# Performance work log

Measured on AMD Instinct MI355X. Metric: run time of the kernel, lower is better.

The kernel has to match this reference:

```python
import jax, jax.numpy as jnp
import numpy as np

B, T, D, H, E, M = 4, 2048, 2048, 8, 512, 8  # batch, seq, hidden, moe_heads, moe_experts, moe_dim//2
F = E * M  # flatten_shape = 4096
HALF = D // 2


def act(z):
    # 'relu2' activation: relu(x)**2
    r = jax.nn.relu(z)
    return r * r


def setup_inputs() -> dict:
    key = jax.random.key(0)
    ks = jax.random.split(key, 13)
    s = 0.02
    return {
        "x": jax.random.normal(ks[0], (B, T, D), jnp.float32),
        "g1": jax.random.uniform(ks[1], (B, T, H, E), jnp.float32),
        "g2": jax.random.uniform(ks[2], (B, T, H, E), jnp.float32),
        "u1_w": jax.random.normal(ks[3], (F, D), jnp.float32) * s,
        "u1_b": jnp.zeros((F,), jnp.float32),
        "u2_w": jax.random.normal(ks[4], (F, D), jnp.float32) * s,
        "u2_b": jnp.zeros((F,), jnp.float32),
        "v11_w": jax.random.normal(ks[5], (HALF, F), jnp.float32) * s,
        "v12_w": jax.random.normal(ks[6], (HALF, F), jnp.float32) * s,
        "v21_w": jax.random.normal(ks[7], (HALF, F), jnp.float32) * s,
        "v22_w": jax.random.normal(ks[8], (HALF, F), jnp.float32) * s,
        "b1": jax.random.normal(ks[9], (E, HALF), jnp.float32) * s,
        "b2": jax.random.normal(ks[10], (E, HALF), jnp.float32) * s,
    }


def reference(x, g1, g2, u1_w, u1_b, u2_w, u2_b, v11_w, v12_w, v21_w, v22_w, b1, b2):
    # x1, x2: [B,T,E,M]
    x1 = act(x @ u1_w.T + u1_b).reshape(B, T, E, M)
    x2 = act(x @ u2_w.T + u2_b).reshape(B, T, E, M)

    g1s = g1.sum(axis=2)  # [B,T,E] (einsum '...hi->...i')
    g2s = g2.sum(axis=2)

    # x11 = v11(einsum('btim,bthi->btim', x1, g1).flatten(-2))
    x11 = (x1 * g1s[..., None]).reshape(B, T, F) @ v11_w.T
    # x12 = v12(einsum('btjm,bthj,bthi->btim', x2, g2, g1).flatten(-2))
    t2 = jnp.einsum('btjm,bthj->bthm', x2, g2)
    x12 = jnp.einsum('bthm,bthi->btim', t2, g1).reshape(B, T, F) @ v12_w.T
    # x13 = einsum('bthi,id->btd', g1, b1)
    x13 = g1s @ b1

    # x21 = v21(einsum('btim,bthi,bthj->btjm', x1, g1, g2).flatten(-2))
    t1 = jnp.einsum('btim,bthi->bthm', x1, g1)
    x21 = jnp.einsum('bthm,bthj->btjm', t1, g2).reshape(B, T, F) @ v21_w.T
    # x22 = v22(einsum('btjm,bthj->btjm', x2, g2).flatten(-2))
    x22 = (x2 * g2s[..., None]).reshape(B, T, F) @ v22_w.T
    # x23 = einsum('bthj,jd->btd', g2, b2)
    x23 = g2s @ b2

    return jnp.concatenate((x11 + x12 + x13, x21 + x22 + x23), axis=-1)
```

## Files before the change

kernel.cpp:

```cpp
#include <hip/hip_runtime.h>
#include <hip/hip_bf16.h>

#define TOK   8192
#define DD    2048
#define FF    4096
#define EE    512
#define HALF  1024
#define KCAT  8704

typedef __bf16 bf16x8 __attribute__((ext_vector_type(8)));
typedef __bf16 bf16x4 __attribute__((ext_vector_type(4)));
typedef float  f32x4  __attribute__((ext_vector_type(4)));
using bf16 = __hip_bfloat16;

#define AS1(p) ((const __attribute__((address_space(1))) void*)(p))
#define AS3(p) ((__attribute__((address_space(3))) void*)(p))


__global__ void cvt_bf16(const float* __restrict__ in, bf16* __restrict__ out, int n4) {
    int i = blockIdx.x * blockDim.x + threadIdx.x;
    int stride = gridDim.x * blockDim.x;
    for (; i < n4; i += stride) {
        float4 v = ((const float4*)in)[i];
        bf16x4 o;
        o[0] = (__bf16)v.x; o[1] = (__bf16)v.y; o[2] = (__bf16)v.z; o[3] = (__bf16)v.w;
        ((bf16x4*)out)[i] = o;
    }
}

__global__ void pack_w(const float* __restrict__ vA, const float* __restrict__ vB,
                       const float* __restrict__ bmat, bf16* __restrict__ W) {
    int n = blockIdx.x;
    const float* ra = vA + (size_t)n * FF;
    const float* rb = vB + (size_t)n * FF;
    bf16* w = W + (size_t)n * KCAT;
    for (int k = threadIdx.x; k < FF; k += 256) {
        w[k]      = __float2bfloat16(ra[k]);
        w[FF + k] = __float2bfloat16(rb[k]);
    }
    for (int e = threadIdx.x; e < EE; e += 256)
        w[2 * FF + e] = __float2bfloat16(bmat[(size_t)e * HALF + n]);
}

template<int MODE>
__global__ __launch_bounds__(512, 2)
void gemmP(const bf16* __restrict__ A0, const bf16* __restrict__ B0,
           const float* __restrict__ bias0, void* __restrict__ C0,
           const bf16* __restrict__ A1, const bf16* __restrict__ B1,
           const float* __restrict__ bias1, void* __restrict__ C1,
           int nbm, int nbn, int K, int ldc)
{
    __shared__ __align__(16) char smem[131072];
    const int tid  = threadIdx.x;
    const int lane = tid & 63;
    const int wid  = tid >> 6;
    const int wm = wid >> 2, wn = wid & 3;
    const int r16 = lane & 15, kb = lane >> 4;

    int bid = blockIdx.x;
    {
        int nwg = gridDim.x;
        int q = nwg >> 3, r = nwg & 7;
        int xcd = bid & 7, idx = bid >> 3;
        bid = (xcd < r ? xcd * (q + 1) : r * (q + 1) + (xcd - r) * q) + idx;
    }
    const int npg = nbm * nbn;
    const int g   = bid / npg;
    const int lb  = bid - g * npg;
    const int bm = lb / nbn, bn = lb - bm * nbn;

    const bf16*  A    = g ? A1 : A0;
    const bf16*  Bw   = g ? B1 : B0;
    const float* bias = g ? bias1 : bias0;
    char* Cout = (char*)(g ? C1 : C0);

    const long row0 = (long)bm * 256;
    const int  col0 = bn * 256;
    const int  nt   = K >> 6;

    const char* gA[2]; const char* gB[2];
    #pragma unroll
    for (int l = 0; l < 2; ++l) {
        const uint32_t S = (uint32_t)(l * 512 + tid) * 16;
        const int r  = (int)(S >> 6);
        const int cb = (int)((S & 63) ^ ((uint32_t)((r >> 1) & 3) << 4));
        gA[l] = (const char*)A  + (row0 + r) * (long)K * 2 + cb;
        gB[l] = (const char*)Bw + (long)(col0 + r) * K * 2 + cb;
    }
    const uint32_t ldst = (uint32_t)(tid & ~63) * 16;

    const uint32_t swz  = ((uint32_t)(r16 >> 1) & 3u) << 4;
    const uint32_t aoff = (uint32_t)((wm * 128 + r16) * 64 + kb * 16) ^ swz;
    const uint32_t boff = (uint32_t)((wn * 64  + r16) * 64 + kb * 16) ^ swz;

    f32x4 acc[8][4];
    #pragma unroll
    for (int i = 0; i < 8; ++i)
        #pragma unroll
        for (int j = 0; j < 4; ++j)
            acc[i][j] = (f32x4){0.f, 0.f, 0.f, 0.f};

    __builtin_amdgcn_global_load_lds(AS1(gA[0]),      AS3(smem +     0 + ldst), 16, 0, 0);
    __builtin_amdgcn_global_load_lds(AS1(gA[1]),      AS3(smem +  8192 + ldst), 16, 0, 0);
    __builtin_amdgcn_global_load_lds(AS1(gB[0]),      AS3(smem + 32768 + ldst), 16, 0, 0);
    __builtin_amdgcn_global_load_lds(AS1(gB[1]),      AS3(smem + 40960 + ldst), 16, 0, 0);
    __builtin_amdgcn_global_load_lds(AS1(gA[0] + 64), AS3(smem + 16384 + ldst), 16, 0, 0);
    __builtin_amdgcn_global_load_lds(AS1(gA[1] + 64), AS3(smem + 24576 + ldst), 16, 0, 0);
    __builtin_amdgcn_global_load_lds(AS1(gB[0] + 64), AS3(smem + 49152 + ldst), 16, 0, 0);
    __builtin_amdgcn_global_load_lds(AS1(gB[1] + 64), AS3(smem + 57344 + ldst), 16, 0, 0);
    asm volatile("s_waitcnt vmcnt(4)\n\ts_barrier" ::: "memory");

#define MFMA16(IH)                                                                       \
    __builtin_amdgcn_s_setprio(1);                                                      \
    _Pragma("unroll")                                                                    \
    for (int fi = 0; fi < 4; ++fi) {                                                     \
        acc[(IH)*4+fi][0] = __builtin_amdgcn_mfma_f32_16x16x32_bf16(af[fi], bv[0], acc[(IH)*4+fi][0], 0, 0, 0); \
        acc[(IH)*4+fi][1] = __builtin_amdgcn_mfma_f32_16x16x32_bf16(af[fi], bv[1], acc[(IH)*4+fi][1], 0, 0, 0); \
        acc[(IH)*4+fi][2] = __builtin_amdgcn_mfma_f32_16x16x32_bf16(af[fi], bv[2], acc[(IH)*4+fi][2], 0, 0, 0); \
        acc[(IH)*4+fi][3] = __builtin_amdgcn_mfma_f32_16x16x32_bf16(af[fi], bv[3], acc[(IH)*4+fi][3], 0, 0, 0); \
    }                                                                                    \
    __builtin_amdgcn_s_setprio(0);

    for (int t = 0; t < nt; ++t) {
        const char* pb = smem + (t & 1) * 65536;
        char*       pt = smem + ((t + 1) & 1) * 65536;
        const bool  st = (t + 1 < nt);
        const long  koff = (long)(t + 1) * 128;

        bf16x8 af[4], bv[4];

        #pragma unroll
        for (int fj = 0; fj < 4; ++fj) bv[fj] = *(const bf16x8*)(pb + 32768 + boff + fj * 1024);
        #pragma unroll
        for (int fi = 0; fi < 4; ++fi) af[fi] = *(const bf16x8*)(pb + aoff + fi * 1024);
        if (st) {
            __builtin_amdgcn_global_load_lds(AS1(gA[0] + koff), AS3(pt +    0 + ldst), 16, 0, 0);
            __builtin_amdgcn_global_load_lds(AS1(gA[1] + koff), AS3(pt + 8192 + ldst), 16, 0, 0);
        }
        asm volatile("s_barrier" ::: "memory");
        MFMA16(0)
        asm volatile("s_barrier" ::: "memory");

        #pragma unroll
        for (int fi = 0; fi < 4; ++fi) af[fi] = *(const bf16x8*)(pb + 4096 + aoff + fi * 1024);
        if (st) {
            __builtin_amdgcn_global_load_lds(AS1(gB[0] + koff), AS3(pt + 32768 + ldst), 16, 0, 0);
            __builtin_amdgcn_global_load_lds(AS1(gB[1] + koff), AS3(pt + 40960 + ldst), 16, 0, 0);
            asm volatile("s_waitcnt vmcnt(4)" ::: "memory");
        } else {
            asm volatile("s_waitcnt vmcnt(0)" ::: "memory");
        }
        asm volatile("s_barrier" ::: "memory");
        MFMA16(1)
        asm volatile("s_barrier" ::: "memory");

        #pragma unroll
        for (int fj = 0; fj < 4; ++fj) bv[fj] = *(const bf16x8*)(pb + 49152 + boff + fj * 1024);
        #pragma unroll
        for (int fi = 0; fi < 4; ++fi) af[fi] = *(const bf16x8*)(pb + 16384 + aoff + fi * 1024);
        if (st) {
            __builtin_amdgcn_global_load_lds(AS1(gA[0] + koff + 64), AS3(pt + 16384 + ldst), 16, 0, 0);
            __builtin_amdgcn_global_load_lds(AS1(gA[1] + koff + 64), AS3(pt + 24576 + ldst), 16, 0, 0);
        }
        asm volatile("s_barrier" ::: "memory");
        MFMA16(0)
        asm volatile("s_barrier" ::: "memory");

        #pragma unroll
        for (int fi = 0; fi < 4; ++fi) af[fi] = *(const bf16x8*)(pb + 16384 + 4096 + aoff + fi * 1024);
        if (st) {
            __builtin_amdgcn_global_load_lds(AS1(gB[0] + koff + 64), AS3(pt + 49152 + ldst), 16, 0, 0);
            __builtin_amdgcn_global_load_lds(AS1(gB[1] + koff + 64), AS3(pt + 57344 + ldst), 16, 0, 0);
            asm volatile("s_waitcnt vmcnt(4)" ::: "memory");
        }
        asm volatile("s_barrier" ::: "memory");
        MFMA16(1)
        asm volatile("s_barrier" ::: "memory");
    }
#undef MFMA16

    const int rb = (lane >> 4) * 4;
    #pragma unroll
    for (int i = 0; i < 8; ++i) {
        #pragma unroll
        for (int j = 0; j < 4; ++j) {
            const int cc = col0 + wn * 64 + j * 16 + r16;
            float badd = 0.f;
            if (MODE == 1) badd = bias[cc];
            #pragma unroll
            for (int e = 0; e < 4; ++e) {
                long row = row0 + wm * 128 + i * 16 + rb + e;
                float v = acc[i][j][e];
                if (MODE == 1) {
                    v += badd;
                    v = fmaxf(v, 0.f);
                    v = v * v;
                    ((bf16*)Cout)[row * ldc + cc] = __float2bfloat16(v);
                } else {
                    ((float*)Cout)[row * ldc + cc] = v;
                }
            }
        }
    }
}

#define GPAD 524
__global__ __launch_bounds__(256)
void glue(const float* __restrict__ g1, const float* __restrict__ g2,
          bf16* __restrict__ Yl, bf16* __restrict__ Yr)
{
    __shared__ __align__(16) float g1t[8 * GPAD];
    __shared__ __align__(16) float g2t[8 * GPAD];
    __shared__ float g1s[EE], g2s[EE];
    __shared__ float t1s[64], t2s[64];
    __shared__ float t1p[4][64], t2p[4][64];
    __shared__ __align__(16) bf16 x1t[FF], x2t[FF];

    const int t   = blockIdx.x;
    const int tid = threadIdx.x;
    const float* g1p = g1 + (size_t)t * FF;
    const float* g2p = g2 + (size_t)t * FF;
    bf16* ylp = Yl + (size_t)t * KCAT;
    bf16* yrp = Yr + (size_t)t * KCAT;

    #pragma unroll
    for (int c = 0; c < 4; ++c) {
        int idx4 = (c * 256 + tid) * 4;
        float4 v1 = *(const float4*)(g1p + idx4);
        float4 v2 = *(const float4*)(g2p + idx4);
        int h = idx4 >> 9, e = idx4 & 511;
        *(float4*)&g1t[h * GPAD + e] = v1;
        *(float4*)&g2t[h * GPAD + e] = v2;
    }
    #pragma unroll
    for (int c = 0; c < 2; ++c) {
        int idx8 = (c * 256 + tid) * 8;
        *(bf16x8*)&x1t[idx8] = *(const bf16x8*)(ylp + idx8);
        *(bf16x8*)&x2t[idx8] = *(const bf16x8*)(yrp + FF + idx8);
    }
    __syncthreads();

    #pragma unroll
    for (int c = 0; c < 2; ++c) {
        int e = c * 256 + tid;
        float s1 = 0.f, s2 = 0.f;
        #pragma unroll
        for (int h = 0; h < 8; ++h) { s1 += g1t[h * GPAD + e]; s2 += g2t[h * GPAD + e]; }
        g1s[e] = s1; g2s[e] = s2;
    }

    {
        int o = tid & 63;
        int h = o & 7, m = o >> 3;
        int p = tid >> 6;
        float s1 = 0.f, s2 = 0.f;
        #pragma unroll 8
        for (int ii = 0; ii < 128; ++ii) {
            int e = p * 128 + ii;
            float xv1 = __bfloat162float(x1t[e * 8 + m]);
            float xv2 = __bfloat162float(x2t[e * 8 + m]);
            s1 += xv1 * g1t[h * GPAD + e];
            s2 += xv2 * g2t[h * GPAD + e];
        }
        t1p[p][o] = s1; t2p[p][o] = s2;
    }
    __syncthreads();
    if (tid < 64)       t1s[tid] = t1p[0][tid] + t1p[1][tid] + t1p[2][tid] + t1p[3][tid];
    else if (tid < 128) { int o = tid - 64; t2s[o] = t2p[0][o] + t2p[1][o] + t2p[2][o] + t2p[3][o]; }
    __syncthreads();

    #pragma unroll
    for (int c = 0; c < 2; ++c) {
        int f0 = (c * 256 + tid) * 8;
        int e  = f0 >> 3;
        float s1 = g1s[e], s2 = g2s[e];
        bf16x8 xa = *(const bf16x8*)&x1t[f0];
        bf16x8 xb = *(const bf16x8*)&x2t[f0];
        bf16x8 o1, o2;
        #pragma unroll
        for (int u = 0; u < 8; ++u) {
            o1[u] = (__bf16)((float)xa[u] * s1);
            o2[u] = (__bf16)((float)xb[u] * s2);
        }
        *(bf16x8*)(ylp + f0)      = o1;
        *(bf16x8*)(yrp + FF + f0) = o2;
    }
    #pragma unroll
    for (int c = 0; c < 2; ++c) {
        int f0 = (c * 256 + tid) * 8;
        int i  = f0 >> 3;
        bf16x8 o12v, o21v;
        #pragma unroll
        for (int m = 0; m < 8; ++m) {
            float s12 = 0.f, s21 = 0.f;
            #pragma unroll
            for (int h = 0; h < 8; ++h) {
                s12 += t2s[(m << 3) | h] * g1t[h * GPAD + i];
                s21 += t1s[(m << 3) | h] * g2t[h * GPAD + i];
            }
            o12v[m] = (__bf16)s12;
            o21v[m] = (__bf16)s21;
        }
        *(bf16x8*)(ylp + FF + f0) = o12v;
        *(bf16x8*)(yrp + f0)      = o21v;
    }
    {
        int e0 = tid * 2;
        ylp[2 * FF + e0]     = __float2bfloat16(g1s[e0]);
        ylp[2 * FF + e0 + 1] = __float2bfloat16(g1s[e0 + 1]);
        yrp[2 * FF + e0]     = __float2bfloat16(g2s[e0]);
        yrp[2 * FF + e0 + 1] = __float2bfloat16(g2s[e0 + 1]);
    }
}


extern "C" void kernel_launch(void* const* d_in, const int* in_sizes, int n_in,
                              void* d_out, int out_size, void* d_ws, size_t ws_size,
                              hipStream_t stream) {
    const float* x    = (const float*)d_in[0];
    const float* g1   = (const float*)d_in[1];
    const float* g2   = (const float*)d_in[2];
    const float* u1_w = (const float*)d_in[3];
    const float* u1_b = (const float*)d_in[4];
    const float* u2_w = (const float*)d_in[5];
    const float* u2_b = (const float*)d_in[6];
    const float* v11  = (const float*)d_in[7];
    const float* v12  = (const float*)d_in[8];
    const float* v21  = (const float*)d_in[9];
    const float* v22  = (const float*)d_in[10];
    const float* b1   = (const float*)d_in[11];
    const float* b2   = (const float*)d_in[12];
    float* out = (float*)d_out;

    size_t off = 0;
    char* base = (char*)d_ws;
    auto take = [&](size_t bytes) { void* p = base + off; off += (bytes + 255) & ~(size_t)255; return p; };
    bf16* Xb  = (bf16*)take((size_t)TOK * DD * 2);
    bf16* U1b = (bf16*)take((size_t)FF * DD * 2);
    bf16* U2b = (bf16*)take((size_t)FF * DD * 2);
    bf16* Wl  = (bf16*)take((size_t)HALF * KCAT * 2);
    bf16* Wr  = (bf16*)take((size_t)HALF * KCAT * 2);
    bf16* Yl  = (bf16*)take((size_t)TOK * KCAT * 2);
    bf16* Yr  = (bf16*)take((size_t)TOK * KCAT * 2);

    cvt_bf16<<<4096, 256, 0, stream>>>(x,    Xb,  TOK * DD / 4);
    cvt_bf16<<<2048, 256, 0, stream>>>(u1_w, U1b, FF * DD / 4);
    cvt_bf16<<<2048, 256, 0, stream>>>(u2_w, U2b, FF * DD / 4);
    pack_w<<<HALF, 256, 0, stream>>>(v11, v12, b1, Wl);
    pack_w<<<HALF, 256, 0, stream>>>(v21, v22, b2, Wr);

    gemmP<1><<<2 * (TOK / 256) * (FF / 256), 512, 0, stream>>>(
        Xb, U1b, u1_b, Yl,
        Xb, U2b, u2_b, Yr + FF,
        TOK / 256, FF / 256, DD, KCAT);

    glue<<<TOK, 256, 0, stream>>>(g1, g2, Yl, Yr);

    gemmP<0><<<2 * (TOK / 256) * (HALF / 256), 512, 0, stream>>>(
        Yl, Wl, nullptr, out,
        Yr, Wr, nullptr, out + HALF,
        TOK / 256, HALF / 256, KCAT, DD);
}
```

Before: 714.4 us.

## Software-pipeline LDS fragment loads against MFMA with double register buffers

The GEMM main loop now keeps two sets of A and B fragment registers. It loads the next sub-tile's fragments from LDS while MFMAs run on the current ones, and prefetches the first fragments of the next K tile at the end of each iteration. This lets it drop the barrier that used to follow each MFMA block, so LDS reads overlap matrix work and fewer sync points stall the waves. The cost is more vector registers in use and a more delicate ordering, since correctness now rests on LDS reads finishing before the async global-to-LDS writes overwrite the same buffer.

```diff
diff --git a/kernel.cpp b/kernel.cpp
--- a/kernel.cpp
+++ b/kernel.cpp
@@ -110,15 +110,22 @@
     __builtin_amdgcn_global_load_lds(AS1(gB[1] + 64), AS3(smem + 57344 + ldst), 16, 0, 0);
     asm volatile("s_waitcnt vmcnt(4)\n\ts_barrier" ::: "memory");
 
-#define MFMA16(IH)                                                                       \
+    bf16x8 afA[4], afB[4], bv0[4], bv1[4];
+    #pragma unroll
+    for (int f = 0; f < 4; ++f) {
+        afA[f] = *(const bf16x8*)(smem +     0 + aoff + f * 1024);
+        bv0[f] = *(const bf16x8*)(smem + 32768 + boff + f * 1024);
+    }
+
+#define MFMA16(AF, BV, IH)                                                              \
     __builtin_amdgcn_s_setprio(1);                                                      \
-    _Pragma("unroll")                                                                    \
-    for (int fi = 0; fi < 4; ++fi) {                                                     \
-        acc[(IH)*4+fi][0] = __builtin_amdgcn_mfma_f32_16x16x32_bf16(af[fi], bv[0], acc[(IH)*4+fi][0], 0, 0, 0); \
-        acc[(IH)*4+fi][1] = __builtin_amdgcn_mfma_f32_16x16x32_bf16(af[fi], bv[1], acc[(IH)*4+fi][1], 0, 0, 0); \
-        acc[(IH)*4+fi][2] = __builtin_amdgcn_mfma_f32_16x16x32_bf16(af[fi], bv[2], acc[(IH)*4+fi][2], 0, 0, 0); \
-        acc[(IH)*4+fi][3] = __builtin_amdgcn_mfma_f32_16x16x32_bf16(af[fi], bv[3], acc[(IH)*4+fi][3], 0, 0, 0); \
-    }                                                                                    \
+    _Pragma("unroll")                                                                   \
+    for (int fi = 0; fi < 4; ++fi) {                                                    \
+        acc[(IH)*4+fi][0] = __builtin_amdgcn_mfma_f32_16x16x32_bf16(AF[fi], BV[0], acc[(IH)*4+fi][0], 0, 0, 0); \
+        acc[(IH)*4+fi][1] = __builtin_amdgcn_mfma_f32_16x16x32_bf16(AF[fi], BV[1], acc[(IH)*4+fi][1], 0, 0, 0); \
+        acc[(IH)*4+fi][2] = __builtin_amdgcn_mfma_f32_16x16x32_bf16(AF[fi], BV[2], acc[(IH)*4+fi][2], 0, 0, 0); \
+        acc[(IH)*4+fi][3] = __builtin_amdgcn_mfma_f32_16x16x32_bf16(AF[fi], BV[3], acc[(IH)*4+fi][3], 0, 0, 0); \
+    }                                                                                   \
     __builtin_amdgcn_s_setprio(0);
 
     for (int t = 0; t < nt; ++t) {
@@ -127,22 +134,16 @@
         const bool  st = (t + 1 < nt);
         const long  koff = (long)(t + 1) * 128;
 
-        bf16x8 af[4], bv[4];
-
-        #pragma unroll
-        for (int fj = 0; fj < 4; ++fj) bv[fj] = *(const bf16x8*)(pb + 32768 + boff + fj * 1024);
-        #pragma unroll
-        for (int fi = 0; fi < 4; ++fi) af[fi] = *(const bf16x8*)(pb + aoff + fi * 1024);
         if (st) {
             __builtin_amdgcn_global_load_lds(AS1(gA[0] + koff), AS3(pt +    0 + ldst), 16, 0, 0);
             __builtin_amdgcn_global_load_lds(AS1(gA[1] + koff), AS3(pt + 8192 + ldst), 16, 0, 0);
         }
         asm volatile("s_barrier" ::: "memory");
-        MFMA16(0)
-        asm volatile("s_barrier" ::: "memory");
-
-        #pragma unroll
-        for (int fi = 0; fi < 4; ++fi) af[fi] = *(const bf16x8*)(pb + 4096 + aoff + fi * 1024);
+        #pragma unroll
+        for (int f = 0; f < 4; ++f)
+            afB[f] = *(const bf16x8*)(pb + 4096 + aoff + f * 1024);
+        MFMA16(afA, bv0, 0)
+
         if (st) {
             __builtin_amdgcn_global_load_lds(AS1(gB[0] + koff), AS3(pt + 32768 + ldst), 16, 0, 0);
             __builtin_amdgcn_global_load_lds(AS1(gB[1] + koff), AS3(pt + 40960 + ldst), 16, 0, 0);
@@ -151,31 +152,37 @@
             asm volatile("s_waitcnt vmcnt(0)" ::: "memory");
         }
         asm volatile("s_barrier" ::: "memory");
-        MFMA16(1)
-        asm volatile("s_barrier" ::: "memory");
-
-        #pragma unroll
-        for (int fj = 0; fj < 4; ++fj) bv[fj] = *(const bf16x8*)(pb + 49152 + boff + fj * 1024);
-        #pragma unroll
-        for (int fi = 0; fi < 4; ++fi) af[fi] = *(const bf16x8*)(pb + 16384 + aoff + fi * 1024);
+        #pragma unroll
+        for (int f = 0; f < 4; ++f) {
+            afA[f] = *(const bf16x8*)(pb + 16384 + aoff + f * 1024);
+            bv1[f] = *(const bf16x8*)(pb + 49152 + boff + f * 1024);
+        }
+        MFMA16(afB, bv0, 1)
+
         if (st) {
             __builtin_amdgcn_global_load_lds(AS1(gA[0] + koff + 64), AS3(pt + 16384 + ldst), 16, 0, 0);
             __builtin_amdgcn_global_load_lds(AS1(gA[1] + koff + 64), AS3(pt + 24576 + ldst), 16, 0, 0);
         }
         asm volatile("s_barrier" ::: "memory");
-        MFMA16(0)
-        asm volatile("s_barrier" ::: "memory");
-
-        #pragma unroll
-        for (int fi = 0; fi < 4; ++fi) af[fi] = *(const bf16x8*)(pb + 16384 + 4096 + aoff + fi * 1024);
+        #pragma unroll
+        for (int f = 0; f < 4; ++f)
+            afB[f] = *(const bf16x8*)(pb + 16384 + 4096 + aoff + f * 1024);
+        MFMA16(afA, bv1, 0)
+
         if (st) {
             __builtin_amdgcn_global_load_lds(AS1(gB[0] + koff + 64), AS3(pt + 49152 + ldst), 16, 0, 0);
             __builtin_amdgcn_global_load_lds(AS1(gB[1] + koff + 64), AS3(pt + 57344 + ldst), 16, 0, 0);
             asm volatile("s_waitcnt vmcnt(4)" ::: "memory");
         }
         asm volatile("s_barrier" ::: "memory");
-        MFMA16(1)
-        asm volatile("s_barrier" ::: "memory");
+        if (st) {
+            #pragma unroll
+            for (int f = 0; f < 4; ++f) {
+                afA[f] = *(const bf16x8*)(pt +     0 + aoff + f * 1024);
+                bv0[f] = *(const bf16x8*)(pt + 32768 + boff + f * 1024);
+            }
+        }
+        MFMA16(afB, bv1, 1)
     }
 #undef MFMA16
 
```

Result: faster. 692.9 us (-3.0%).

## Restructure GEMM main loop with 128-byte K rows and staggered prefetch

Applied to the files above, without the earlier changes.

Replaces the GEMM inner loop. LDS tiles now hold a full 64-wide K slice per row (128 bytes) with an 8-way XOR swizzle, and each wave covers a 128x64 quadrant split differently. Global-to-LDS staging for the next tiles is spread across the four MFMA phases, some two iterations ahead, with explicit lgkmcnt waits and sched barriers. Launch bounds drop from 2 to 1 blocks per CU to give the compiler more registers. This aims to cut LDS bank conflicts and overlap memory with compute better, at the cost of occupancy and more complex synchronisation.

```diff
diff --git a/kernel.cpp b/kernel.cpp
--- a/kernel.cpp
+++ b/kernel.cpp
@@ -43,8 +43,8 @@
 }
 
 template<int MODE>
-__global__ __launch_bounds__(512, 2)
-void gemmP(const bf16* __restrict__ A0, const bf16* __restrict__ B0,
+__global__ __launch_bounds__(512, 1)
+void gemmQ(const bf16* __restrict__ A0, const bf16* __restrict__ B0,
            const float* __restrict__ bias0, void* __restrict__ C0,
            const bf16* __restrict__ A1, const bf16* __restrict__ B1,
            const float* __restrict__ bias1, void* __restrict__ C1,
@@ -78,20 +78,31 @@
     const int  col0 = bn * 256;
     const int  nt   = K >> 6;
 
-    const char* gA[2]; const char* gB[2];
+    const char* sA[2][2]; const char* sB[2][2];
     #pragma unroll
     for (int l = 0; l < 2; ++l) {
         const uint32_t S = (uint32_t)(l * 512 + tid) * 16;
-        const int r  = (int)(S >> 6);
-        const int cb = (int)((S & 63) ^ ((uint32_t)((r >> 1) & 3) << 4));
-        gA[l] = (const char*)A  + (row0 + r) * (long)K * 2 + cb;
-        gB[l] = (const char*)Bw + (long)(col0 + r) * K * 2 + cb;
-    }
-    const uint32_t ldst = (uint32_t)(tid & ~63) * 16;
-
-    const uint32_t swz  = ((uint32_t)(r16 >> 1) & 3u) << 4;
-    const uint32_t aoff = (uint32_t)((wm * 128 + r16) * 64 + kb * 16) ^ swz;
-    const uint32_t boff = (uint32_t)((wn * 64  + r16) * 64 + kb * 16) ^ swz;
+        const int r  = (int)(S >> 7);
+        const int cs = (int)((S & 127) ^ (((uint32_t)r & 7) << 4));
+        sA[0][l] = (const char*)A  + (row0 + r)       * (long)K * 2 + cs;
+        sA[1][l] = (const char*)A  + (row0 + 128 + r) * (long)K * 2 + cs;
+        sB[0][l] = (const char*)Bw + (long)(col0 + r)       * K * 2 + cs;
+        sB[1][l] = (const char*)Bw + (long)(col0 + 128 + r) * K * 2 + cs;
+    }
+    const uint32_t dst0 = (uint32_t)(tid & ~63) * 16;
+
+#define STAGE(SP, BASE, KOFF)                                                            \
+    __builtin_amdgcn_global_load_lds(AS1(SP[0] + (KOFF)), AS3(smem + (BASE) + dst0), 16, 0, 0); \
+    __builtin_amdgcn_global_load_lds(AS1(SP[1] + (KOFF)), AS3(smem + (BASE) + 8192 + dst0), 16, 0, 0);
+
+    const uint32_t sw = ((uint32_t)(r16 & 7)) << 4;
+    uint32_t co[2];
+    co[0] = ((uint32_t)(kb * 16)) ^ sw;
+    co[1] = ((uint32_t)(64 + kb * 16)) ^ sw;
+    const uint32_t arow = (uint32_t)(r16 * 128);
+    const uint32_t brow = (uint32_t)(((wn & 1) * 64 + r16) * 128);
+    const uint32_t Ab = (uint32_t)wm * 16384u;
+    const uint32_t Bb = 32768u + ((uint32_t)(wn >> 1)) * 16384u;
 
     f32x4 acc[8][4];
     #pragma unroll
@@ -100,84 +111,90 @@
         for (int j = 0; j < 4; ++j)
             acc[i][j] = (f32x4){0.f, 0.f, 0.f, 0.f};
 
-    __builtin_amdgcn_global_load_lds(AS1(gA[0]),      AS3(smem +     0 + ldst), 16, 0, 0);
-    __builtin_amdgcn_global_load_lds(AS1(gA[1]),      AS3(smem +  8192 + ldst), 16, 0, 0);
-    __builtin_amdgcn_global_load_lds(AS1(gB[0]),      AS3(smem + 32768 + ldst), 16, 0, 0);
-    __builtin_amdgcn_global_load_lds(AS1(gB[1]),      AS3(smem + 40960 + ldst), 16, 0, 0);
-    __builtin_amdgcn_global_load_lds(AS1(gA[0] + 64), AS3(smem + 16384 + ldst), 16, 0, 0);
-    __builtin_amdgcn_global_load_lds(AS1(gA[1] + 64), AS3(smem + 24576 + ldst), 16, 0, 0);
-    __builtin_amdgcn_global_load_lds(AS1(gB[0] + 64), AS3(smem + 49152 + ldst), 16, 0, 0);
-    __builtin_amdgcn_global_load_lds(AS1(gB[1] + 64), AS3(smem + 57344 + ldst), 16, 0, 0);
-    asm volatile("s_waitcnt vmcnt(4)\n\ts_barrier" ::: "memory");
-
-#define MFMA16(IH)                                                                       \
+    STAGE(sA[0],     0, 0) STAGE(sB[0], 32768, 0) STAGE(sA[1], 16384, 0) STAGE(sB[1], 49152, 0)
+    if (nt > 1) {
+        STAGE(sA[0], 65536 +     0, 128) STAGE(sB[0], 65536 + 32768, 128) STAGE(sB[1], 65536 + 49152, 128)
+        asm volatile("s_waitcnt vmcnt(6)" ::: "memory");
+    } else {
+        asm volatile("s_waitcnt vmcnt(0)" ::: "memory");
+    }
+    asm volatile("s_barrier" ::: "memory");
+
+#define QUAD(RO, CO, AF, BV)                                                            \
     __builtin_amdgcn_s_setprio(1);                                                      \
-    _Pragma("unroll")                                                                    \
-    for (int fi = 0; fi < 4; ++fi) {                                                     \
-        acc[(IH)*4+fi][0] = __builtin_amdgcn_mfma_f32_16x16x32_bf16(af[fi], bv[0], acc[(IH)*4+fi][0], 0, 0, 0); \
-        acc[(IH)*4+fi][1] = __builtin_amdgcn_mfma_f32_16x16x32_bf16(af[fi], bv[1], acc[(IH)*4+fi][1], 0, 0, 0); \
-        acc[(IH)*4+fi][2] = __builtin_amdgcn_mfma_f32_16x16x32_bf16(af[fi], bv[2], acc[(IH)*4+fi][2], 0, 0, 0); \
-        acc[(IH)*4+fi][3] = __builtin_amdgcn_mfma_f32_16x16x32_bf16(af[fi], bv[3], acc[(IH)*4+fi][3], 0, 0, 0); \
-    }                                                                                    \
+    _Pragma("unroll")                                                                   \
+    for (int f = 0; f < 4; ++f) {                                                       \
+        _Pragma("unroll")                                                               \
+        for (int j = 0; j < 2; ++j) {                                                   \
+            acc[(RO)+f][(CO)+j] = __builtin_amdgcn_mfma_f32_16x16x32_bf16(AF[0][f], BV[0][j], acc[(RO)+f][(CO)+j], 0, 0, 0); \
+            acc[(RO)+f][(CO)+j] = __builtin_amdgcn_mfma_f32_16x16x32_bf16(AF[1][f], BV[1][j], acc[(RO)+f][(CO)+j], 0, 0, 0); \
+        }                                                                               \
+    }                                                                                   \
     __builtin_amdgcn_s_setprio(0);
 
+#define LGKM0()                                                                         \
+    asm volatile("s_waitcnt lgkmcnt(0)" ::: "memory");                                  \
+    __builtin_amdgcn_sched_barrier(0);
+
+    bf16x8 af[2][4], bv[2][2], bv2[2][2];
+
     for (int t = 0; t < nt; ++t) {
-        const char* pb = smem + (t & 1) * 65536;
-        char*       pt = smem + ((t + 1) & 1) * 65536;
-        const bool  st = (t + 1 < nt);
-        const long  koff = (long)(t + 1) * 128;
-
-        bf16x8 af[4], bv[4];
-
-        #pragma unroll
-        for (int fj = 0; fj < 4; ++fj) bv[fj] = *(const bf16x8*)(pb + 32768 + boff + fj * 1024);
-        #pragma unroll
-        for (int fi = 0; fi < 4; ++fi) af[fi] = *(const bf16x8*)(pb + aoff + fi * 1024);
-        if (st) {
-            __builtin_amdgcn_global_load_lds(AS1(gA[0] + koff), AS3(pt +    0 + ldst), 16, 0, 0);
-            __builtin_amdgcn_global_load_lds(AS1(gA[1] + koff), AS3(pt + 8192 + ldst), 16, 0, 0);
-        }
-        asm volatile("s_barrier" ::: "memory");
-        MFMA16(0)
-        asm volatile("s_barrier" ::: "memory");
-
-        #pragma unroll
-        for (int fi = 0; fi < 4; ++fi) af[fi] = *(const bf16x8*)(pb + 4096 + aoff + fi * 1024);
-        if (st) {
-            __builtin_amdgcn_global_load_lds(AS1(gB[0] + koff), AS3(pt + 32768 + ldst), 16, 0, 0);
-            __builtin_amdgcn_global_load_lds(AS1(gB[1] + koff), AS3(pt + 40960 + ldst), 16, 0, 0);
-            asm volatile("s_waitcnt vmcnt(4)" ::: "memory");
-        } else {
+        const uint32_t bo  = ((uint32_t)(t & 1)) << 16;
+        const uint32_t bo1 = bo ^ 65536u;
+        const char* pb = smem + bo;
+        const long k1 = (long)(t + 1) * 128;
+        const long k2 = (long)(t + 2) * 128;
+
+        #pragma unroll
+        for (int kk = 0; kk < 2; ++kk) {
+            #pragma unroll
+            for (int f = 0; f < 4; ++f)
+                af[kk][f] = *(const bf16x8*)(pb + Ab + arow + f * 2048 + co[kk]);
+            #pragma unroll
+            for (int j = 0; j < 2; ++j)
+                bv[kk][j] = *(const bf16x8*)(pb + Bb + brow + j * 2048 + co[kk]);
+        }
+        if (t + 1 < nt) { STAGE(sA[1], bo1 + 16384, k1) }
+        asm volatile("s_barrier" ::: "memory");
+        LGKM0()
+        QUAD(0, 0, af, bv)
+        asm volatile("s_barrier" ::: "memory");
+
+        #pragma unroll
+        for (int kk = 0; kk < 2; ++kk)
+            #pragma unroll
+            for (int j = 0; j < 2; ++j)
+                bv2[kk][j] = *(const bf16x8*)(pb + Bb + brow + (j + 2) * 2048 + co[kk]);
+        asm volatile("s_barrier" ::: "memory");
+        LGKM0()
+        QUAD(0, 2, af, bv2)
+        asm volatile("s_barrier" ::: "memory");
+
+        #pragma unroll
+        for (int kk = 0; kk < 2; ++kk)
+            #pragma unroll
+            for (int f = 0; f < 4; ++f)
+                af[kk][f] = *(const bf16x8*)(pb + Ab + arow + (f + 4) * 2048 + co[kk]);
+        if (t + 2 < nt) { STAGE(sB[0], bo + 32768, k2) }
+        asm volatile("s_barrier" ::: "memory");
+        LGKM0()
+        QUAD(4, 0, af, bv)
+        asm volatile("s_barrier" ::: "memory");
+
+        if (t + 2 < nt) {
+            STAGE(sA[0], bo, k2) STAGE(sB[1], bo + 49152, k2)
+            asm volatile("s_waitcnt vmcnt(6)" ::: "memory");
+        } else if (t + 1 < nt) {
             asm volatile("s_waitcnt vmcnt(0)" ::: "memory");
         }
         asm volatile("s_barrier" ::: "memory");
-        MFMA16(1)
-        asm volatile("s_barrier" ::: "memory");
-
-        #pragma unroll
-        for (int fj = 0; fj < 4; ++fj) bv[fj] = *(const bf16x8*)(pb + 49152 + boff + fj * 1024);
-        #pragma unroll
-        for (int fi = 0; fi < 4; ++fi) af[fi] = *(const bf16x8*)(pb + 16384 + aoff + fi * 1024);
-        if (st) {
-            __builtin_amdgcn_global_load_lds(AS1(gA[0] + koff + 64), AS3(pt + 16384 + ldst), 16, 0, 0);
-            __builtin_amdgcn_global_load_lds(AS1(gA[1] + koff + 64), AS3(pt + 24576 + ldst), 16, 0, 0);
-        }
-        asm volatile("s_barrier" ::: "memory");
-        MFMA16(0)
-        asm volatile("s_barrier" ::: "memory");
-
-        #pragma unroll
-        for (int fi = 0; fi < 4; ++fi) af[fi] = *(const bf16x8*)(pb + 16384 + 4096 + aoff + fi * 1024);
-        if (st) {
-            __builtin_amdgcn_global_load_lds(AS1(gB[0] + koff + 64), AS3(pt + 49152 + ldst), 16, 0, 0);
-            __builtin_amdgcn_global_load_lds(AS1(gB[1] + koff + 64), AS3(pt + 57344 + ldst), 16, 0, 0);
-            asm volatile("s_waitcnt vmcnt(4)" ::: "memory");
-        }
-        asm volatile("s_barrier" ::: "memory");
-        MFMA16(1)
-        asm volatile("s_barrier" ::: "memory");
-    }
-#undef MFMA16
+        __builtin_amdgcn_sched_barrier(0);
+        QUAD(4, 2, af, bv2)
+        asm volatile("s_barrier" ::: "memory");
+    }
+#undef QUAD
+#undef LGKM0
+#undef STAGE
 
     const int rb = (lane >> 4) * 4;
     #pragma unroll
@@ -349,14 +366,14 @@
     pack_w<<<HALF, 256, 0, stream>>>(v11, v12, b1, Wl);
     pack_w<<<HALF, 256, 0, stream>>>(v21, v22, b2, Wr);
 
-    gemmP<1><<<2 * (TOK / 256) * (FF / 256), 512, 0, stream>>>(
+    gemmQ<1><<<2 * (TOK / 256) * (FF / 256), 512, 0, stream>>>(
         Xb, U1b, u1_b, Yl,
         Xb, U2b, u2_b, Yr + FF,
         TOK / 256, FF / 256, DD, KCAT);
 
     glue<<<TOK, 256, 0, stream>>>(g1, g2, Yl, Yr);
 
-    gemmP<0><<<2 * (TOK / 256) * (HALF / 256), 512, 0, stream>>>(
+    gemmQ<0><<<2 * (TOK / 256) * (HALF / 256), 512, 0, stream>>>(
         Yl, Wl, nullptr, out,
         Yr, Wr, nullptr, out + HALF,
         TOK / 256, HALF / 256, KCAT, DD);
```

New measurement: 678.9 us. 1.05x faster.

## Restructure GEMM main loop into register double-buffered LDS reads with fewer barriers

Applied to the files above, without the earlier changes.

Rewrites the GEMM K-loop so each 64-wide K half-tile is read from LDS into a full 8x4 fragment set (af/bv double-buffered in registers). The next half-tile's LDS reads are issued before the MFMA block on the current one, which cuts the per-iteration barrier count from eight to two. The aim is to hide LDS latency behind MFMAs and reduce synchronisation stalls. In exchange it holds twice as many fragment registers, which could raise VGPR pressure at 512 threads with launch bounds of 2 blocks per CU.

```diff
diff --git a/kernel.cpp b/kernel.cpp
--- a/kernel.cpp
+++ b/kernel.cpp
@@ -44,7 +44,7 @@
 
 template<int MODE>
 __global__ __launch_bounds__(512, 2)
-void gemmP(const bf16* __restrict__ A0, const bf16* __restrict__ B0,
+void gemmR(const bf16* __restrict__ A0, const bf16* __restrict__ B0,
            const float* __restrict__ bias0, void* __restrict__ C0,
            const bf16* __restrict__ A1, const bf16* __restrict__ B1,
            const float* __restrict__ bias1, void* __restrict__ C1,
@@ -100,84 +100,61 @@
         for (int j = 0; j < 4; ++j)
             acc[i][j] = (f32x4){0.f, 0.f, 0.f, 0.f};
 
-    __builtin_amdgcn_global_load_lds(AS1(gA[0]),      AS3(smem +     0 + ldst), 16, 0, 0);
-    __builtin_amdgcn_global_load_lds(AS1(gA[1]),      AS3(smem +  8192 + ldst), 16, 0, 0);
-    __builtin_amdgcn_global_load_lds(AS1(gB[0]),      AS3(smem + 32768 + ldst), 16, 0, 0);
-    __builtin_amdgcn_global_load_lds(AS1(gB[1]),      AS3(smem + 40960 + ldst), 16, 0, 0);
-    __builtin_amdgcn_global_load_lds(AS1(gA[0] + 64), AS3(smem + 16384 + ldst), 16, 0, 0);
-    __builtin_amdgcn_global_load_lds(AS1(gA[1] + 64), AS3(smem + 24576 + ldst), 16, 0, 0);
-    __builtin_amdgcn_global_load_lds(AS1(gB[0] + 64), AS3(smem + 49152 + ldst), 16, 0, 0);
-    __builtin_amdgcn_global_load_lds(AS1(gB[1] + 64), AS3(smem + 57344 + ldst), 16, 0, 0);
-    asm volatile("s_waitcnt vmcnt(4)\n\ts_barrier" ::: "memory");
-
-#define MFMA16(IH)                                                                       \
-    __builtin_amdgcn_s_setprio(1);                                                      \
+#define STAGEK(BUFOFF, KOFF)                                                             \
+    __builtin_amdgcn_global_load_lds(AS1(gA[0] + (KOFF)), AS3(smem + (BUFOFF) +     0 + ldst), 16, 0, 0); \
+    __builtin_amdgcn_global_load_lds(AS1(gA[1] + (KOFF)), AS3(smem + (BUFOFF) +  8192 + ldst), 16, 0, 0); \
+    __builtin_amdgcn_global_load_lds(AS1(gB[0] + (KOFF)), AS3(smem + (BUFOFF) + 32768 + ldst), 16, 0, 0); \
+    __builtin_amdgcn_global_load_lds(AS1(gB[1] + (KOFF)), AS3(smem + (BUFOFF) + 40960 + ldst), 16, 0, 0);
+
+#define READS(AF, BV, PB, PLOFF)                                                         \
     _Pragma("unroll")                                                                    \
-    for (int fi = 0; fi < 4; ++fi) {                                                     \
-        acc[(IH)*4+fi][0] = __builtin_amdgcn_mfma_f32_16x16x32_bf16(af[fi], bv[0], acc[(IH)*4+fi][0], 0, 0, 0); \
-        acc[(IH)*4+fi][1] = __builtin_amdgcn_mfma_f32_16x16x32_bf16(af[fi], bv[1], acc[(IH)*4+fi][1], 0, 0, 0); \
-        acc[(IH)*4+fi][2] = __builtin_amdgcn_mfma_f32_16x16x32_bf16(af[fi], bv[2], acc[(IH)*4+fi][2], 0, 0, 0); \
-        acc[(IH)*4+fi][3] = __builtin_amdgcn_mfma_f32_16x16x32_bf16(af[fi], bv[3], acc[(IH)*4+fi][3], 0, 0, 0); \
+    for (int fi = 0; fi < 8; ++fi) AF[fi] = *(const bf16x8*)((PB) + (PLOFF) + aoff + fi * 1024); \
+    _Pragma("unroll")                                                                    \
+    for (int fj = 0; fj < 4; ++fj) BV[fj] = *(const bf16x8*)((PB) + (PLOFF) + 32768 + boff + fj * 1024);
+
+#define MFMA32(AF, BV)                                                                   \
+    __builtin_amdgcn_s_setprio(1);                                                       \
+    _Pragma("unroll")                                                                    \
+    for (int fi = 0; fi < 8; ++fi) {                                                     \
+        _Pragma("unroll")                                                                \
+        for (int fj = 0; fj < 4; ++fj)                                                   \
+            acc[fi][fj] = __builtin_amdgcn_mfma_f32_16x16x32_bf16(AF[fi], BV[fj], acc[fi][fj], 0, 0, 0); \
     }                                                                                    \
     __builtin_amdgcn_s_setprio(0);
 
+    STAGEK(0, 0)
+    STAGEK(16384, 64)
+    asm volatile("s_waitcnt vmcnt(4)\n\ts_barrier" ::: "memory");
+
+    bf16x8 af0[8], bv0[4], af1[8], bv1[4];
+    READS(af0, bv0, smem, 0)
+
     for (int t = 0; t < nt; ++t) {
-        const char* pb = smem + (t & 1) * 65536;
-        char*       pt = smem + ((t + 1) & 1) * 65536;
+        const uint32_t bo  = ((uint32_t)(t & 1)) << 16;
+        const uint32_t bo1 = bo ^ 65536u;
+        const char* pb = smem + bo;
+        const char* pt = smem + bo1;
         const bool  st = (t + 1 < nt);
-        const long  koff = (long)(t + 1) * 128;
-
-        bf16x8 af[4], bv[4];
-
-        #pragma unroll
-        for (int fj = 0; fj < 4; ++fj) bv[fj] = *(const bf16x8*)(pb + 32768 + boff + fj * 1024);
-        #pragma unroll
-        for (int fi = 0; fi < 4; ++fi) af[fi] = *(const bf16x8*)(pb + aoff + fi * 1024);
+        const long  k1 = (long)(t + 1) * 128;
+
+        if (st) { STAGEK(bo1, k1) }
+        if (st) asm volatile("s_waitcnt vmcnt(4)" ::: "memory");
+        else    asm volatile("s_waitcnt vmcnt(0)" ::: "memory");
+        asm volatile("s_barrier" ::: "memory");
+        READS(af1, bv1, pb, 16384)
+        MFMA32(af0, bv0)
+
         if (st) {
-            __builtin_amdgcn_global_load_lds(AS1(gA[0] + koff), AS3(pt +    0 + ldst), 16, 0, 0);
-            __builtin_amdgcn_global_load_lds(AS1(gA[1] + koff), AS3(pt + 8192 + ldst), 16, 0, 0);
+            STAGEK(bo1 + 16384, k1 + 64)
+            asm volatile("s_waitcnt vmcnt(4)" ::: "memory");
         }
         asm volatile("s_barrier" ::: "memory");
-        MFMA16(0)
-        asm volatile("s_barrier" ::: "memory");
-
-        #pragma unroll
-        for (int fi = 0; fi < 4; ++fi) af[fi] = *(const bf16x8*)(pb + 4096 + aoff + fi * 1024);
-        if (st) {
-            __builtin_amdgcn_global_load_lds(AS1(gB[0] + koff), AS3(pt + 32768 + ldst), 16, 0, 0);
-            __builtin_amdgcn_global_load_lds(AS1(gB[1] + koff), AS3(pt + 40960 + ldst), 16, 0, 0);
-            asm volatile("s_waitcnt vmcnt(4)" ::: "memory");
-        } else {
-            asm volatile("s_waitcnt vmcnt(0)" ::: "memory");
-        }
-        asm volatile("s_barrier" ::: "memory");
-        MFMA16(1)
-        asm volatile("s_barrier" ::: "memory");
-
-        #pragma unroll
-        for (int fj = 0; fj < 4; ++fj) bv[fj] = *(const bf16x8*)(pb + 49152 + boff + fj * 1024);
-        #pragma unroll
-        for (int fi = 0; fi < 4; ++fi) af[fi] = *(const bf16x8*)(pb + 16384 + aoff + fi * 1024);
-        if (st) {
-            __builtin_amdgcn_global_load_lds(AS1(gA[0] + koff + 64), AS3(pt + 16384 + ldst), 16, 0, 0);
-            __builtin_amdgcn_global_load_lds(AS1(gA[1] + koff + 64), AS3(pt + 24576 + ldst), 16, 0, 0);
-        }
-        asm volatile("s_barrier" ::: "memory");
-        MFMA16(0)
-        asm volatile("s_barrier" ::: "memory");
-
-        #pragma unroll
-        for (int fi = 0; fi < 4; ++fi) af[fi] = *(const bf16x8*)(pb + 16384 + 4096 + aoff + fi * 1024);
-        if (st) {
-            __builtin_amdgcn_global_load_lds(AS1(gB[0] + koff + 64), AS3(pt + 49152 + ldst), 16, 0, 0);
-            __builtin_amdgcn_global_load_lds(AS1(gB[1] + koff + 64), AS3(pt + 57344 + ldst), 16, 0, 0);
-            asm volatile("s_waitcnt vmcnt(4)" ::: "memory");
-        }
-        asm volatile("s_barrier" ::: "memory");
-        MFMA16(1)
-        asm volatile("s_barrier" ::: "memory");
-    }
-#undef MFMA16
+        if (st) { READS(af0, bv0, pt, 0) }
+        MFMA32(af1, bv1)
+    }
+#undef MFMA32
+#undef READS
+#undef STAGEK
 
     const int rb = (lane >> 4) * 4;
     #pragma unroll
@@ -349,14 +326,14 @@
     pack_w<<<HALF, 256, 0, stream>>>(v11, v12, b1, Wl);
     pack_w<<<HALF, 256, 0, stream>>>(v21, v22, b2, Wr);
 
-    gemmP<1><<<2 * (TOK / 256) * (FF / 256), 512, 0, stream>>>(
+    gemmR<1><<<2 * (TOK / 256) * (FF / 256), 512, 0, stream>>>(
         Xb, U1b, u1_b, Yl,
         Xb, U2b, u2_b, Yr + FF,
         TOK / 256, FF / 256, DD, KCAT);
 
     glue<<<TOK, 256, 0, stream>>>(g1, g2, Yl, Yr);
 
-    gemmP<0><<<2 * (TOK / 256) * (HALF / 256), 512, 0, stream>>>(
+    gemmR<0><<<2 * (TOK / 256) * (HALF / 256), 512, 0, stream>>>(
         Yl, Wl, nullptr, out,
         Yr, Wr, nullptr, out + HALF,
         TOK / 256, HALF / 256, KCAT, DD);
```

Measured after the change: 726.7 us. About the same (+1.7%).
